# Performance work log

Hardware: AMD Instinct MI355X
Metric: run time of the kernel (lower is better)

## Reference

```python
import jax, jax.numpy as jnp
import numpy as np

EMBED_DIM = 1024
NUM_HEADS = 16
HEAD_DIM = EMBED_DIM // NUM_HEADS


def setup_inputs() -> dict:
    key = jax.random.key(0)
    k1, k2, k3 = jax.random.split(key, 3)
    scale = 1.0 / np.sqrt(EMBED_DIM)
    x = jax.random.normal(k1, (2, 2048, EMBED_DIM), dtype=jnp.float32)
    w_qkv = jax.random.normal(k2, (EMBED_DIM, 3 * EMBED_DIM), dtype=jnp.float32) * scale
    b_qkv = jnp.zeros((3 * EMBED_DIM,), dtype=jnp.float32)
    w_out = jax.random.normal(k3, (EMBED_DIM, EMBED_DIM), dtype=jnp.float32) * scale
    b_out = jnp.zeros((EMBED_DIM,), dtype=jnp.float32)
    return {"x": x, "w_qkv": w_qkv, "b_qkv": b_qkv, "w_out": w_out, "b_out": b_out}


def reference(x, w_qkv, b_qkv, w_out, b_out):
    B, N, C = x.shape
    H, D = NUM_HEADS, HEAD_DIM
    qkv = x @ w_qkv + b_qkv                      # [B, N, 3C]
    qkv = qkv.reshape(B, N, 3, H, D)
    q = qkv[:, :, 0].transpose(0, 2, 1, 3)       # [B, H, N, D]
    k = qkv[:, :, 1].transpose(0, 2, 1, 3)
    v = qkv[:, :, 2].transpose(0, 2, 1, 3)
    scores = jnp.einsum('bhnd,bhmd->bhnm', q, k) / jnp.sqrt(jnp.float32(D))
    attn = jax.nn.softmax(scores, axis=-1)
    out = jnp.einsum('bhnm,bhmd->bhnd', attn, v)  # [B, H, N, D]
    out = out.transpose(0, 2, 1, 3).reshape(B, N, C)
    return out @ w_out + b_out
```

## Files before the change

kernel.cpp:

```cpp
#include <hip/hip_runtime.h>
#include <stdint.h>

typedef unsigned short u16;
typedef short s16x8 __attribute__((ext_vector_type(8)));
typedef unsigned short u16x8 __attribute__((ext_vector_type(8)));
typedef unsigned short u16x4 __attribute__((ext_vector_type(4)));
typedef float f32x4 __attribute__((ext_vector_type(4)));
typedef float f32x16 __attribute__((ext_vector_type(16)));
typedef unsigned int u32x2 __attribute__((ext_vector_type(2)));

#if __has_builtin(__builtin_amdgcn_exp2f)
#define EXP2F(x) __builtin_amdgcn_exp2f(x)
#else
#define EXP2F(x) exp2f(x)
#endif

#define QSCALE 0.18033688011112042f

__device__ __forceinline__ u16 f2b(float f) {
  union { float f; uint32_t u; } v; v.f = f;
  uint32_t r = (v.u + 0x7fffu + ((v.u >> 16) & 1u)) >> 16;
  return (u16)r;
}

__device__ __forceinline__ uint32_t pkhi(uint32_t hi, uint32_t lo) {
#if __has_builtin(__builtin_amdgcn_perm)
  return __builtin_amdgcn_perm(hi, lo, 0x07060302u);
#else
  return (lo >> 16) | (hi & 0xffff0000u);
#endif
}

__device__ __forceinline__ void gld16(const void* g, void* l) {
  __builtin_amdgcn_global_load_lds((__attribute__((address_space(1))) void*)g,
                                   (__attribute__((address_space(3))) void*)l,
                                   16, 0, 0);
}

__global__ __launch_bounds__(256)
void cast_bf16(const float* __restrict__ src, u16* __restrict__ dst) {
  const size_t i = ((size_t)blockIdx.x * 256 + threadIdx.x) * 8;
  f32x4 v0 = *(const f32x4*)(src + i);
  f32x4 v1 = *(const f32x4*)(src + i + 4);
  u16x8 u;
#pragma unroll
  for (int j = 0; j < 4; j++) { u[j] = f2b(v0[j]); u[4 + j] = f2b(v1[j]); }
  *(u16x8*)(dst + i) = u;
}

__global__ __launch_bounds__(256)
void transpose_cast(const float* __restrict__ src, u16* __restrict__ dst,
                    int K, int N) {
  __shared__ float tile[32][33];
  const int nb = blockIdx.x * 32, kb = blockIdx.y * 32;
  const int tx = threadIdx.x, ty = threadIdx.y;
#pragma unroll
  for (int i = 0; i < 4; i++)
    tile[ty + i * 8][tx] = src[(size_t)(kb + ty + i * 8) * N + nb + tx];
  __syncthreads();
#pragma unroll
  for (int i = 0; i < 4; i++)
    dst[(size_t)(nb + ty + i * 8) * K + kb + tx] = f2b(tile[tx][ty + i * 8]);
}

template <int EPI>
__global__ __launch_bounds__(256)
void gemm_bt(const u16* __restrict__ A, const u16* __restrict__ Bt,
             const float* __restrict__ bias, float* __restrict__ outF,
             u16* __restrict__ outQ, u16* __restrict__ outK,
             u16* __restrict__ outVt, int M, int N, int K) {
  __shared__ char smem[34816];
  u16* As = (u16*)smem;
  u16* Bs = As + 128 * 32;

  const int t = threadIdx.x;
  const int m0 = blockIdx.y * 128, n0 = blockIdx.x * 128;
  const int w = t >> 6, lane = t & 63;
  const int wm = w >> 1, wn = w & 1;
  const int quad = lane >> 4, lrow = lane & 15;
  const int srow = lane >> 2, scol = (lane & 3) * 8;

  f32x4 acc[4][4];
#pragma unroll
  for (int i = 0; i < 4; i++)
#pragma unroll
    for (int j = 0; j < 4; j++) {
      f32x4 z = {0.f, 0.f, 0.f, 0.f};
      acc[i][j] = z;
    }

  for (int k0 = 0; k0 < K; k0 += 32) {
    __syncthreads();
    {
      const u16* ga = A + (size_t)(m0 + w * 32 + srow) * K + k0 + scol;
      gld16(ga, &As[(w * 32) * 32]);
      gld16(ga + (size_t)16 * K, &As[(w * 32 + 16) * 32]);
      const u16* gb = Bt + (size_t)(n0 + w * 32 + srow) * K + k0 + scol;
      gld16(gb, &Bs[(w * 32) * 32]);
      gld16(gb + (size_t)16 * K, &Bs[(w * 32 + 16) * 32]);
    }
    __syncthreads();

    s16x8 a[4], b[4];
#pragma unroll
    for (int i = 0; i < 4; i++)
      a[i] = *(const s16x8*)&As[(wm * 64 + i * 16 + lrow) * 32 + quad * 8];
#pragma unroll
    for (int j = 0; j < 4; j++)
      b[j] = *(const s16x8*)&Bs[(wn * 64 + j * 16 + lrow) * 32 + quad * 8];
#pragma unroll
    for (int i = 0; i < 4; i++)
#pragma unroll
      for (int j = 0; j < 4; j++)
        acc[i][j] =
            __builtin_amdgcn_mfma_f32_16x16x32_bf16(a[i], b[j], acc[i][j], 0, 0, 0);
  }

  if (EPI == 1) {
#pragma unroll
    for (int i = 0; i < 4; i++) {
      const int row = m0 + wm * 64 + i * 16 + quad * 4;
#pragma unroll
      for (int j = 0; j < 4; j++) {
        const int col = n0 + wn * 64 + j * 16 + lrow;
        const float bv = bias[col];
#pragma unroll
        for (int r = 0; r < 4; r++)
          outF[(size_t)(row + r) * N + col] = acc[i][j][r] + bv;
      }
    }
    return;
  }

  __syncthreads();
  u16* rp = (u16*)smem + w * (64 * 68);
  const int cb = n0 + wn * 64;
  const int which = cb >> 10;
  const int h = (cb & 1023) >> 6;
  const int rbase = m0 + wm * 64;
  const int bb = rbase >> 11, nn0 = rbase & 2047;
  const int rl = lane >> 3, cc = (lane & 7) * 8;

  if (which != 2) {
    const float s = (which == 0) ? QSCALE : 1.0f;
#pragma unroll
    for (int i = 0; i < 4; i++)
#pragma unroll
      for (int j = 0; j < 4; j++) {
        const float bv = bias[cb + j * 16 + lrow];
#pragma unroll
        for (int r = 0; r < 4; r++)
          rp[(i * 16 + quad * 4 + r) * 68 + j * 16 + lrow] =
              f2b((acc[i][j][r] + bv) * s);
      }
    u16* dst = ((which == 0) ? outQ : outK) +
               ((size_t)(bb * 16 + h) * 2048 + nn0) * 64;
#pragma unroll
    for (int it = 0; it < 8; it++) {
      const int row = it * 8 + rl;
      *(u16x8*)&dst[(size_t)row * 64 + cc] = *(const u16x8*)&rp[row * 68 + cc];
    }
  } else {
#pragma unroll
    for (int i = 0; i < 4; i++)
#pragma unroll
      for (int j = 0; j < 4; j++) {
        const float bv = bias[cb + j * 16 + lrow];
        u16x4 pk;
#pragma unroll
        for (int r = 0; r < 4; r++) pk[r] = f2b(acc[i][j][r] + bv);
        *(u16x4*)&rp[(j * 16 + lrow) * 68 + i * 16 + quad * 4] = pk;
      }
    u16* dst = outVt + ((size_t)(bb * 16 + h) * 64) * 2048 + nn0;
#pragma unroll
    for (int it = 0; it < 8; it++) {
      const int d = it * 8 + rl;
      *(u16x8*)&dst[(size_t)d * 2048 + cc] = *(const u16x8*)&rp[d * 68 + cc];
    }
  }
}

__global__ __launch_bounds__(256)
void attn_kernel(const u16* __restrict__ Q, const u16* __restrict__ Kg,
                 const u16* __restrict__ Vt, u16* __restrict__ AO) {
  __shared__ u16 Ks[64 * 64];
  __shared__ u16 Vs[64 * 64];
  __shared__ u16 Pt[4][32 * 72];

  const int t = threadIdx.x;
  const int bh = blockIdx.x;
  const int qt = blockIdx.y;
  const int w = t >> 6, lane = t & 63;
  const int l31 = lane & 31, lh = lane >> 5, l7 = lane & 7;
  const int srow8 = lane >> 3, chunk = lane & 7;
  const int csw = chunk ^ srow8;
  const size_t base = (size_t)bh * 2048 * 64;

  s16x8 qf[4];
  {
    const u16* qp = Q + base + (size_t)(qt * 128 + w * 32 + l31) * 64 + lh * 8;
#pragma unroll
    for (int ks = 0; ks < 4; ks++) qf[ks] = *(const s16x8*)(qp + ks * 16);
  }

  int cx[4];
#pragma unroll
  for (int ks = 0; ks < 4; ks++) cx[ks] = ((2 * ks + lh) ^ l7) * 8;

  const u16* kgl = Kg + base + (size_t)(w * 16 + srow8) * 64 + csw * 8;
  const u16* vgl = Vt + base + (size_t)(w * 16 + srow8) * 2048 + csw * 8;
  u16* kls = &Ks[(w * 16) * 64];
  u16* vls = &Vs[(w * 16) * 64];

  f32x16 ot0, ot1;
#pragma unroll
  for (int e = 0; e < 16; e++) { ot0[e] = 0.f; ot1[e] = 0.f; }
  float li = 0.f;

  for (int kt = 0; kt < 32; kt++) {
    __syncthreads();
    gld16(kgl + (size_t)kt * 4096, kls);
    gld16(kgl + (size_t)kt * 4096 + 512, kls + 512);
    gld16(vgl + kt * 64, vls);
    gld16(vgl + kt * 64 + (size_t)8 * 2048, vls + 512);
    __syncthreads();

    f32x16 sc0, sc1;
#pragma unroll
    for (int e = 0; e < 16; e++) { sc0[e] = 0.f; sc1[e] = 0.f; }
#pragma unroll
    for (int ks = 0; ks < 4; ks++) {
      s16x8 k0 = *(const s16x8*)&Ks[l31 * 64 + cx[ks]];
      s16x8 k1 = *(const s16x8*)&Ks[(32 + l31) * 64 + cx[ks]];
      sc0 = __builtin_amdgcn_mfma_f32_32x32x16_bf16(k0, qf[ks], sc0, 0, 0, 0);
      sc1 = __builtin_amdgcn_mfma_f32_32x32x16_bf16(k1, qf[ks], sc1, 0, 0, 0);
    }

    u16* prow = &Pt[w][l31 * 72];
    float rsum = 0.f;
#pragma unroll
    for (int tb = 0; tb < 2; tb++) {
      const f32x16& s = tb ? sc1 : sc0;
#pragma unroll
      for (int g = 0; g < 4; g++) {
        uint32_t u[4];
#pragma unroll
        for (int r = 0; r < 4; r++) {
          float p = EXP2F(s[g * 4 + r]);
          u[r] = __builtin_bit_cast(uint32_t, p);
          rsum += __builtin_bit_cast(float, u[r] & 0xffff0000u);
        }
        u32x2 pk;
        pk[0] = pkhi(u[1], u[0]);
        pk[1] = pkhi(u[3], u[2]);
        *(u32x2*)(prow + tb * 32 + g * 8 + lh * 4) = pk;
      }
    }
    li += rsum;

#pragma unroll
    for (int ks = 0; ks < 4; ks++) {
      s16x8 pf = *(const s16x8*)(prow + ks * 16 + lh * 8);
      s16x8 v0 = *(const s16x8*)&Vs[l31 * 64 + cx[ks]];
      s16x8 v1 = *(const s16x8*)&Vs[(32 + l31) * 64 + cx[ks]];
      ot0 = __builtin_amdgcn_mfma_f32_32x32x16_bf16(v0, pf, ot0, 0, 0, 0);
      ot1 = __builtin_amdgcn_mfma_f32_32x32x16_bf16(v1, pf, ot1, 0, 0, 0);
    }
  }

  li += __shfl_xor(li, 32);
  const float inv = 1.0f / li;
  const int bb = bh >> 4, h = bh & 15;
  const int qn = qt * 128 + w * 32 + l31;
  u16* dst = AO + (size_t)(bb * 2048 + qn) * 1024 + h * 64;
#pragma unroll
  for (int db = 0; db < 2; db++) {
    const f32x16& o = db ? ot1 : ot0;
#pragma unroll
    for (int g = 0; g < 4; g++) {
      const int d0 = db * 32 + g * 8 + lh * 4;
      u16x4 pk;
#pragma unroll
      for (int r = 0; r < 4; r++) pk[r] = f2b(o[g * 4 + r] * inv);
      *(u16x4*)&dst[d0] = pk;
    }
  }
}

extern "C" void kernel_launch(void* const* d_in, const int* in_sizes, int n_in,
                              void* d_out, int out_size, void* d_ws,
                              size_t ws_size, hipStream_t stream) {
  const float* x     = (const float*)d_in[0];
  const float* w_qkv = (const float*)d_in[1];
  const float* b_qkv = (const float*)d_in[2];
  const float* w_out = (const float*)d_in[3];
  const float* b_out = (const float*)d_in[4];
  float* out = (float*)d_out;

  char* ws = (char*)d_ws;
  u16* wqT = (u16*)ws; ws += (size_t)3072 * 1024 * 2;
  u16* woT = (u16*)ws; ws += (size_t)1024 * 1024 * 2;
  u16* q   = (u16*)ws; ws += (size_t)32 * 2048 * 64 * 2;
  u16* k   = (u16*)ws; ws += (size_t)32 * 2048 * 64 * 2;
  u16* vt  = (u16*)ws; ws += (size_t)32 * 64 * 2048 * 2;
  u16* xb  = (u16*)ws; ws += (size_t)4096 * 1024 * 2;
  u16* ao  = xb;

  cast_bf16<<<dim3(2048), 256, 0, stream>>>(x, xb);
  transpose_cast<<<dim3(96, 32), dim3(32, 8), 0, stream>>>(w_qkv, wqT, 1024, 3072);
  transpose_cast<<<dim3(32, 32), dim3(32, 8), 0, stream>>>(w_out, woT, 1024, 1024);
  gemm_bt<0><<<dim3(24, 32), 256, 0, stream>>>(xb, wqT, b_qkv, nullptr, q, k, vt,
                                               4096, 3072, 1024);
  attn_kernel<<<dim3(32, 16), 256, 0, stream>>>(q, k, vt, ao);
  gemm_bt<1><<<dim3(8, 32), 256, 0, stream>>>(ao, woT, b_out, out, nullptr,
                                              nullptr, nullptr, 4096, 1024, 1024);
}
```

Baseline: 215.7 us.

## Register-prefetch GEMM and attention tiles, widen K-step, shrink attention and out-proj blocks

Replaces global_load_lds direct loads with register prefetching: each iteration stores the previously loaded tile to swizzled LDS, then issues the next tile's global loads before the compute barrier, so loads overlap MFMA work. The GEMM K-step doubles to 64 with an XOR swizzle, and it gains a WN template so the output projection uses 128x64 tiles with more blocks. Attention blocks shrink to 2 waves of 64 queries, doubling the grid. exp2 moves from the amdgcn builtin to exp2f. Costs are higher register pressure, and the exp2f swap may add instructions.

```diff
diff --git a/kernel.cpp b/kernel.cpp
--- a/kernel.cpp
+++ b/kernel.cpp
@@ -9,12 +9,7 @@
 typedef float f32x16 __attribute__((ext_vector_type(16)));
 typedef unsigned int u32x2 __attribute__((ext_vector_type(2)));
 
-#if __has_builtin(__builtin_amdgcn_exp2f)
-#define EXP2F(x) __builtin_amdgcn_exp2f(x)
-#else
 #define EXP2F(x) exp2f(x)
-#endif
-
 #define QSCALE 0.18033688011112042f
 
 __device__ __forceinline__ u16 f2b(float f) {
@@ -31,10 +26,8 @@
 #endif
 }
 
-__device__ __forceinline__ void gld16(const void* g, void* l) {
-  __builtin_amdgcn_global_load_lds((__attribute__((address_space(1))) void*)g,
-                                   (__attribute__((address_space(3))) void*)l,
-                                   16, 0, 0);
+__device__ __forceinline__ void sync_lds() {
+  asm volatile("s_waitcnt lgkmcnt(0)\ns_barrier" ::: "memory");
 }
 
 __global__ __launch_bounds__(256)
@@ -63,63 +56,91 @@
     dst[(size_t)(nb + ty + i * 8) * K + kb + tx] = f2b(tile[tx][ty + i * 8]);
 }
 
-template <int EPI>
-__global__ __launch_bounds__(256)
+template <int EPI, int WN>
+__global__ __launch_bounds__(256, 3)
 void gemm_bt(const u16* __restrict__ A, const u16* __restrict__ Bt,
              const float* __restrict__ bias, float* __restrict__ outF,
              u16* __restrict__ outQ, u16* __restrict__ outK,
              u16* __restrict__ outVt, int M, int N, int K) {
-  __shared__ char smem[34816];
+  constexpr int BN = WN * 64;
+  constexpr int RW = 4 / WN;
+  constexpr int MI = 128 / RW / 16;
+  constexpr int NBI = WN * 2;
+  constexpr int SMEM = (EPI == 0) ? 34816 : (16384 + WN * 8192);
+  __shared__ char smem[SMEM];
   u16* As = (u16*)smem;
-  u16* Bs = As + 128 * 32;
+  u16* Bs = As + 128 * 64;
 
   const int t = threadIdx.x;
-  const int m0 = blockIdx.y * 128, n0 = blockIdx.x * 128;
+  const int m0 = blockIdx.y * 128, n0 = blockIdx.x * BN;
   const int w = t >> 6, lane = t & 63;
-  const int wm = w >> 1, wn = w & 1;
+  const int wm = w / WN, wn = w % WN;
   const int quad = lane >> 4, lrow = lane & 15;
-  const int srow = lane >> 2, scol = (lane & 3) * 8;
-
-  f32x4 acc[4][4];
-#pragma unroll
-  for (int i = 0; i < 4; i++)
+  const int r8 = lane >> 3, s8 = lane & 7;
+  const int csw = (s8 ^ r8) * 8;
+
+  const u16* gA = A + (size_t)(m0 + w * 32 + r8) * K + csw;
+  const u16* gB = Bt + (size_t)(n0 + w * (WN * 16) + r8) * K + csw;
+  u16* wAs = As + (w * 32 + r8) * 64 + s8 * 8;
+  u16* wBs = Bs + (w * (WN * 16) + r8) * 64 + s8 * 8;
+
+  f32x4 acc[MI][4];
+#pragma unroll
+  for (int i = 0; i < MI; i++)
 #pragma unroll
     for (int j = 0; j < 4; j++) {
       f32x4 z = {0.f, 0.f, 0.f, 0.f};
       acc[i][j] = z;
     }
 
-  for (int k0 = 0; k0 < K; k0 += 32) {
-    __syncthreads();
-    {
-      const u16* ga = A + (size_t)(m0 + w * 32 + srow) * K + k0 + scol;
-      gld16(ga, &As[(w * 32) * 32]);
-      gld16(ga + (size_t)16 * K, &As[(w * 32 + 16) * 32]);
-      const u16* gb = Bt + (size_t)(n0 + w * 32 + srow) * K + k0 + scol;
-      gld16(gb, &Bs[(w * 32) * 32]);
-      gld16(gb + (size_t)16 * K, &Bs[(w * 32 + 16) * 32]);
-    }
-    __syncthreads();
-
-    s16x8 a[4], b[4];
-#pragma unroll
-    for (int i = 0; i < 4; i++)
-      a[i] = *(const s16x8*)&As[(wm * 64 + i * 16 + lrow) * 32 + quad * 8];
-#pragma unroll
-    for (int j = 0; j < 4; j++)
-      b[j] = *(const s16x8*)&Bs[(wn * 64 + j * 16 + lrow) * 32 + quad * 8];
-#pragma unroll
-    for (int i = 0; i < 4; i++)
+  u16x8 pa[4], pb[NBI];
+#pragma unroll
+  for (int i = 0; i < 4; i++) pa[i] = *(const u16x8*)(gA + (size_t)(i * 8) * K);
+#pragma unroll
+  for (int i = 0; i < NBI; i++) pb[i] = *(const u16x8*)(gB + (size_t)(i * 8) * K);
+
+  const int KT = K >> 6;
+  for (int kt = 0; kt < KT; ++kt) {
+    sync_lds();
+#pragma unroll
+    for (int i = 0; i < 4; i++) *(u16x8*)(wAs + i * 8 * 64) = pa[i];
+#pragma unroll
+    for (int i = 0; i < NBI; i++) *(u16x8*)(wBs + i * 8 * 64) = pb[i];
+    if (kt + 1 < KT) {
+      const size_t off = (size_t)(kt + 1) * 64;
+#pragma unroll
+      for (int i = 0; i < 4; i++)
+        pa[i] = *(const u16x8*)(gA + (size_t)(i * 8) * K + off);
+#pragma unroll
+      for (int i = 0; i < NBI; i++)
+        pb[i] = *(const u16x8*)(gB + (size_t)(i * 8) * K + off);
+    }
+    sync_lds();
+
+#pragma unroll
+    for (int ks = 0; ks < 2; ks++) {
+      s16x8 a[MI], b[4];
+#pragma unroll
+      for (int i = 0; i < MI; i++)
+        a[i] = *(const s16x8*)&As[(wm * (MI * 16) + i * 16 + lrow) * 64 +
+                                  (((ks * 4 + quad) ^ (lrow & 7)) * 8)];
 #pragma unroll
       for (int j = 0; j < 4; j++)
-        acc[i][j] =
-            __builtin_amdgcn_mfma_f32_16x16x32_bf16(a[i], b[j], acc[i][j], 0, 0, 0);
+        b[j] = *(const s16x8*)&Bs[(wn * 64 + j * 16 + lrow) * 64 +
+                                  (((ks * 4 + quad) ^ (lrow & 7)) * 8)];
+#pragma unroll
+      for (int i = 0; i < MI; i++)
+#pragma unroll
+        for (int j = 0; j < 4; j++)
+          acc[i][j] = __builtin_amdgcn_mfma_f32_16x16x32_bf16(a[i], b[j],
+                                                              acc[i][j], 0, 0, 0);
+    }
   }
 
   if (EPI == 1) {
 #pragma unroll
-    for (int i = 0; i < 4; i++) {
-      const int row = m0 + wm * 64 + i * 16 + quad * 4;
+    for (int i = 0; i < MI; i++) {
+      const int row = m0 + wm * (MI * 16) + i * 16 + quad * 4;
 #pragma unroll
       for (int j = 0; j < 4; j++) {
         const int col = n0 + wn * 64 + j * 16 + lrow;
@@ -132,7 +153,7 @@
     return;
   }
 
-  __syncthreads();
+  sync_lds();
   u16* rp = (u16*)smem + w * (64 * 68);
   const int cb = n0 + wn * 64;
   const int which = cb >> 10;
@@ -180,37 +201,40 @@
   }
 }
 
-__global__ __launch_bounds__(256)
+__global__ __launch_bounds__(128)
 void attn_kernel(const u16* __restrict__ Q, const u16* __restrict__ Kg,
                  const u16* __restrict__ Vt, u16* __restrict__ AO) {
   __shared__ u16 Ks[64 * 64];
   __shared__ u16 Vs[64 * 64];
-  __shared__ u16 Pt[4][32 * 72];
+  __shared__ u16 Pt[2][32 * 72];
 
   const int t = threadIdx.x;
   const int bh = blockIdx.x;
   const int qt = blockIdx.y;
   const int w = t >> 6, lane = t & 63;
-  const int l31 = lane & 31, lh = lane >> 5, l7 = lane & 7;
-  const int srow8 = lane >> 3, chunk = lane & 7;
-  const int csw = chunk ^ srow8;
+  const int l31 = lane & 31, lh = lane >> 5;
+  const int r8 = lane >> 3, s8 = lane & 7;
+  const int csw = (s8 ^ r8) * 8;
   const size_t base = (size_t)bh * 2048 * 64;
 
   s16x8 qf[4];
   {
-    const u16* qp = Q + base + (size_t)(qt * 128 + w * 32 + l31) * 64 + lh * 8;
+    const u16* qp = Q + base + (size_t)(qt * 64 + w * 32 + l31) * 64 + lh * 8;
 #pragma unroll
     for (int ks = 0; ks < 4; ks++) qf[ks] = *(const s16x8*)(qp + ks * 16);
   }
 
-  int cx[4];
-#pragma unroll
-  for (int ks = 0; ks < 4; ks++) cx[ks] = ((2 * ks + lh) ^ l7) * 8;
-
-  const u16* kgl = Kg + base + (size_t)(w * 16 + srow8) * 64 + csw * 8;
-  const u16* vgl = Vt + base + (size_t)(w * 16 + srow8) * 2048 + csw * 8;
-  u16* kls = &Ks[(w * 16) * 64];
-  u16* vls = &Vs[(w * 16) * 64];
+  const u16* gK = Kg + base + (size_t)(w * 32 + r8) * 64 + csw;
+  const u16* gV = Vt + base + (size_t)(w * 32 + r8) * 2048 + csw;
+  u16* wK = Ks + (w * 32 + r8) * 64 + s8 * 8;
+  u16* wV = Vs + (w * 32 + r8) * 64 + s8 * 8;
+
+  u16x8 pk_[4], pv_[4];
+#pragma unroll
+  for (int i = 0; i < 4; i++) {
+    pk_[i] = *(const u16x8*)(gK + (size_t)(i * 8) * 64);
+    pv_[i] = *(const u16x8*)(gV + (size_t)(i * 8) * 2048);
+  }
 
   f32x16 ot0, ot1;
 #pragma unroll
@@ -218,20 +242,31 @@
   float li = 0.f;
 
   for (int kt = 0; kt < 32; kt++) {
-    __syncthreads();
-    gld16(kgl + (size_t)kt * 4096, kls);
-    gld16(kgl + (size_t)kt * 4096 + 512, kls + 512);
-    gld16(vgl + kt * 64, vls);
-    gld16(vgl + kt * 64 + (size_t)8 * 2048, vls + 512);
-    __syncthreads();
+    sync_lds();
+#pragma unroll
+    for (int i = 0; i < 4; i++) {
+      *(u16x8*)(wK + i * 8 * 64) = pk_[i];
+      *(u16x8*)(wV + i * 8 * 64) = pv_[i];
+    }
+    if (kt + 1 < 32) {
+      const u16* nK = gK + (size_t)(kt + 1) * 64 * 64;
+      const u16* nV = gV + (kt + 1) * 64;
+#pragma unroll
+      for (int i = 0; i < 4; i++) {
+        pk_[i] = *(const u16x8*)(nK + (size_t)(i * 8) * 64);
+        pv_[i] = *(const u16x8*)(nV + (size_t)(i * 8) * 2048);
+      }
+    }
+    sync_lds();
 
     f32x16 sc0, sc1;
 #pragma unroll
     for (int e = 0; e < 16; e++) { sc0[e] = 0.f; sc1[e] = 0.f; }
 #pragma unroll
     for (int ks = 0; ks < 4; ks++) {
-      s16x8 k0 = *(const s16x8*)&Ks[l31 * 64 + cx[ks]];
-      s16x8 k1 = *(const s16x8*)&Ks[(32 + l31) * 64 + cx[ks]];
+      const int sl = (((2 * ks + lh) ^ (l31 & 7)) * 8);
+      s16x8 k0 = *(const s16x8*)&Ks[l31 * 64 + sl];
+      s16x8 k1 = *(const s16x8*)&Ks[(32 + l31) * 64 + sl];
       sc0 = __builtin_amdgcn_mfma_f32_32x32x16_bf16(k0, qf[ks], sc0, 0, 0, 0);
       sc1 = __builtin_amdgcn_mfma_f32_32x32x16_bf16(k1, qf[ks], sc1, 0, 0, 0);
     }
@@ -260,9 +295,10 @@
 
 #pragma unroll
     for (int ks = 0; ks < 4; ks++) {
+      const int sl = (((2 * ks + lh) ^ (l31 & 7)) * 8);
       s16x8 pf = *(const s16x8*)(prow + ks * 16 + lh * 8);
-      s16x8 v0 = *(const s16x8*)&Vs[l31 * 64 + cx[ks]];
-      s16x8 v1 = *(const s16x8*)&Vs[(32 + l31) * 64 + cx[ks]];
+      s16x8 v0 = *(const s16x8*)&Vs[l31 * 64 + sl];
+      s16x8 v1 = *(const s16x8*)&Vs[(32 + l31) * 64 + sl];
       ot0 = __builtin_amdgcn_mfma_f32_32x32x16_bf16(v0, pf, ot0, 0, 0, 0);
       ot1 = __builtin_amdgcn_mfma_f32_32x32x16_bf16(v1, pf, ot1, 0, 0, 0);
     }
@@ -271,18 +307,17 @@
   li += __shfl_xor(li, 32);
   const float inv = 1.0f / li;
   const int bb = bh >> 4, h = bh & 15;
-  const int qn = qt * 128 + w * 32 + l31;
+  const int qn = qt * 64 + w * 32 + l31;
   u16* dst = AO + (size_t)(bb * 2048 + qn) * 1024 + h * 64;
 #pragma unroll
   for (int db = 0; db < 2; db++) {
     const f32x16& o = db ? ot1 : ot0;
 #pragma unroll
     for (int g = 0; g < 4; g++) {
-      const int d0 = db * 32 + g * 8 + lh * 4;
       u16x4 pk;
 #pragma unroll
       for (int r = 0; r < 4; r++) pk[r] = f2b(o[g * 4 + r] * inv);
-      *(u16x4*)&dst[d0] = pk;
+      *(u16x4*)&dst[db * 32 + g * 8 + lh * 4] = pk;
     }
   }
 }
@@ -309,9 +344,9 @@
   cast_bf16<<<dim3(2048), 256, 0, stream>>>(x, xb);
   transpose_cast<<<dim3(96, 32), dim3(32, 8), 0, stream>>>(w_qkv, wqT, 1024, 3072);
   transpose_cast<<<dim3(32, 32), dim3(32, 8), 0, stream>>>(w_out, woT, 1024, 1024);
-  gemm_bt<0><<<dim3(24, 32), 256, 0, stream>>>(xb, wqT, b_qkv, nullptr, q, k, vt,
-                                               4096, 3072, 1024);
-  attn_kernel<<<dim3(32, 16), 256, 0, stream>>>(q, k, vt, ao);
-  gemm_bt<1><<<dim3(8, 32), 256, 0, stream>>>(ao, woT, b_out, out, nullptr,
-                                              nullptr, nullptr, 4096, 1024, 1024);
-}
+  gemm_bt<0, 2><<<dim3(24, 32), 256, 0, stream>>>(xb, wqT, b_qkv, nullptr, q, k,
+                                                  vt, 4096, 3072, 1024);
+  attn_kernel<<<dim3(32, 32), 128, 0, stream>>>(q, k, vt, ao);
+  gemm_bt<1, 1><<<dim3(16, 32), 256, 0, stream>>>(ao, woT, b_out, out, nullptr,
+                                                  nullptr, nullptr, 4096, 1024, 1024);
+}
```

Result: no change. 219.4 us (+1.7%).
